# Optimization experiments

Measured on AMD Instinct MI355X. Metric: run time of the kernel, lower is better.

## Reference

```python
import jax, jax.numpy as jnp
import numpy as np

K1, K2 = 2, 4  # kernels of the two channel groups
BN_EPS = 1e-5


def _neocell_group(x, wa, wb, k):
    # Block-diagonal (a @ x) @ b with a k x k block repeated along the diagonal
    # per channel (NeoCellRepeat): equivalent to blockwise transforms on H and W.
    B, c, H, W = x.shape
    xb = x.reshape(B, c, H // k, k, W // k, k)
    y = jnp.einsum('cpi,bcnimj,cjq->bcnpmq', wa, xb, wb)
    return y.reshape(B, c, H, W)


def setup_inputs() -> dict:
    key = jax.random.key(0)
    ks = jax.random.split(key, 12)
    B, C, H, W = 32, 256, 56, 56
    c1, c2 = 128, 128
    Ci = 4 * C  # inner_mult = 4
    x = jax.random.normal(ks[0], (B, C, H, W), dtype=jnp.float32)
    wa1 = jax.random.normal(ks[1], (c1, K1, K1), dtype=jnp.float32) / np.float32(np.sqrt(K1))
    wb1 = jax.random.normal(ks[2], (c1, K1, K1), dtype=jnp.float32) / np.float32(np.sqrt(K1))
    wa2 = jax.random.normal(ks[3], (c2, K2, K2), dtype=jnp.float32) / np.float32(np.sqrt(K2))
    wb2 = jax.random.normal(ks[4], (c2, K2, K2), dtype=jnp.float32) / np.float32(np.sqrt(K2))
    bn_weight = 1.0 + 0.1 * jax.random.normal(ks[5], (C,), dtype=jnp.float32)
    bn_bias = 0.1 * jax.random.normal(ks[6], (C,), dtype=jnp.float32)
    bn_mean = 0.1 * jax.random.normal(ks[7], (C,), dtype=jnp.float32)
    bn_var = jax.random.uniform(ks[8], (C,), dtype=jnp.float32, minval=0.5, maxval=1.5)
    fc1_w = jax.random.normal(ks[9], (Ci, C), dtype=jnp.float32) / np.float32(np.sqrt(C))
    fc2_w = jax.random.normal(ks[10], (C, Ci), dtype=jnp.float32) / np.float32(np.sqrt(Ci))
    return {"x": x, "wa1": wa1, "wb1": wb1, "wa2": wa2, "wb2": wb2,
            "bn_weight": bn_weight, "bn_bias": bn_bias, "bn_mean": bn_mean,
            "bn_var": bn_var, "fc1_w": fc1_w, "fc2_w": fc2_w}


def reference(x, wa1, wb1, wa2, wb2, bn_weight, bn_bias, bn_mean, bn_var, fc1_w, fc2_w):
    c1 = wa1.shape[0]
    # NeoCell: per-group block-diagonal (a @ x) @ b
    y = jnp.concatenate([
        _neocell_group(x[:, :c1], wa1, wb1, K1),
        _neocell_group(x[:, c1:], wa2, wb2, K2),
    ], axis=1)
    # BatchNorm2d (eval mode, running stats)
    inv = jax.lax.rsqrt(bn_var + BN_EPS)
    scale = (bn_weight * inv)[None, :, None, None]
    shift = (bn_bias - bn_mean * bn_weight * inv)[None, :, None, None]
    y = y * scale + shift
    # chw -> hwc, MLP with exact GELU, hwc -> chw
    y = jnp.transpose(y, (0, 2, 3, 1))
    h = jax.nn.gelu(y @ fc1_w.T, approximate=False)
    y = h @ fc2_w.T
    y = jnp.transpose(y, (0, 3, 1, 2))
    # residual (drop_path = 0)
    return y + x
```

## Files before the change

### kernel.cpp

```cpp
#include <hip/hip_runtime.h>
#include <stdint.h>

typedef __bf16 bf16x8 __attribute__((ext_vector_type(8)));
typedef float f32x4 __attribute__((ext_vector_type(4)));

__device__ __forceinline__ float bf2f(uint16_t u) {
  union { uint32_t i; float f; } v; v.i = ((uint32_t)u) << 16; return v.f;
}
__device__ __forceinline__ uint16_t f2bf(float f) {
  union { float f; uint32_t i; } v; v.f = f;
  uint32_t u = v.i;
  uint32_t r = (u + 0x7FFFu + ((u >> 16) & 1u)) >> 16;
  return (uint16_t)r;
}

__global__ __launch_bounds__(256) void cvt_weights_kernel(
    const float* __restrict__ fc1, const float* __restrict__ fc2,
    uint16_t* __restrict__ fc1b, uint16_t* __restrict__ fc2b)
{
  int i = (blockIdx.x * 256 + threadIdx.x) * 4;
  if (i < 262144) {
    float4 a = *(const float4*)(fc1 + i);
    ushort4 o;
    o.x = f2bf(a.x); o.y = f2bf(a.y); o.z = f2bf(a.z); o.w = f2bf(a.w);
    *(ushort4*)(fc1b + i) = o;
  } else {
    int j = i - 262144;
    float4 a = *(const float4*)(fc2 + j);
    ushort4 o;
    o.x = f2bf(a.x); o.y = f2bf(a.y); o.z = f2bf(a.z); o.w = f2bf(a.w);
    *(ushort4*)(fc2b + j) = o;
  }
}

__global__ __launch_bounds__(128) void neocell_bn_kernel(
    const float* __restrict__ x,
    const float* __restrict__ wa1, const float* __restrict__ wb1,
    const float* __restrict__ wa2, const float* __restrict__ wb2,
    const float* __restrict__ bnw, const float* __restrict__ bnb,
    const float* __restrict__ bnm, const float* __restrict__ bnv,
    uint16_t* __restrict__ y1)
{
  __shared__ uint16_t lx[128 * 226];
  const int t = threadIdx.x;
  const int strip = blockIdx.x;
  const int b = blockIdx.y;
  const int half = blockIdx.z;
  const int h0 = strip * 4;

  for (int i = 0; i < 56; ++i) {
    int l = t + i * 128;
    int c = l / 56;
    int r = l - c * 56;
    const float* g = x + (size_t)(b * 256 + half * 128 + c) * 3136
                       + h0 * 56 + r * 4;
    float4 v = *(const float4*)g;
    ushort4 o;
    o.x = f2bf(v.x); o.y = f2bf(v.y); o.z = f2bf(v.z); o.w = f2bf(v.w);
    *(ushort4*)(lx + c * 226 + r * 4) = o;
  }
  __syncthreads();

  const int c = half * 128 + t;
  const float scale = bnw[c] * rsqrtf(bnv[c] + 1e-5f);
  const float shift = bnb[c] - bnm[c] * scale;
  const uint16_t* lc = lx + t * 226;
  const size_t prow0 = (size_t)b * 56;

  if (half == 0) {
    float A[2][2], Bm[2][2];
#pragma unroll
    for (int p = 0; p < 2; ++p)
#pragma unroll
      for (int i = 0; i < 2; ++i) A[p][i] = wa1[t * 4 + p * 2 + i];
#pragma unroll
    for (int j = 0; j < 2; ++j)
#pragma unroll
      for (int q = 0; q < 2; ++q) Bm[j][q] = wb1[t * 4 + j * 2 + q];

    for (int n2 = 0; n2 < 2; ++n2) {
      for (int m = 0; m < 28; ++m) {
        float X[2][2], T[2][2];
#pragma unroll
        for (int i = 0; i < 2; ++i)
#pragma unroll
          for (int j = 0; j < 2; ++j)
            X[i][j] = bf2f(lc[(n2 * 2 + i) * 56 + m * 2 + j]);
#pragma unroll
        for (int p = 0; p < 2; ++p)
#pragma unroll
          for (int j = 0; j < 2; ++j)
            T[p][j] = A[p][0] * X[0][j] + A[p][1] * X[1][j];
#pragma unroll
        for (int p = 0; p < 2; ++p)
#pragma unroll
          for (int q = 0; q < 2; ++q) {
            float v = T[p][0] * Bm[0][q] + T[p][1] * Bm[1][q];
            v = v * scale + shift;
            size_t pix = (prow0 + h0 + n2 * 2 + p) * 56 + (m * 2 + q);
            y1[pix * 256 + c] = f2bf(v);
          }
      }
    }
  } else {
    float A[4][4], Bm[4][4];
#pragma unroll
    for (int p = 0; p < 4; ++p)
#pragma unroll
      for (int i = 0; i < 4; ++i) A[p][i] = wa2[t * 16 + p * 4 + i];
#pragma unroll
    for (int j = 0; j < 4; ++j)
#pragma unroll
      for (int q = 0; q < 4; ++q) Bm[j][q] = wb2[t * 16 + j * 4 + q];

    for (int m = 0; m < 14; ++m) {
      float X[4][4], T[4][4];
#pragma unroll
      for (int i = 0; i < 4; ++i)
#pragma unroll
        for (int j = 0; j < 4; ++j)
          X[i][j] = bf2f(lc[i * 56 + m * 4 + j]);
#pragma unroll
      for (int p = 0; p < 4; ++p)
#pragma unroll
        for (int j = 0; j < 4; ++j)
          T[p][j] = A[p][0] * X[0][j] + A[p][1] * X[1][j]
                  + A[p][2] * X[2][j] + A[p][3] * X[3][j];
#pragma unroll
      for (int p = 0; p < 4; ++p)
#pragma unroll
        for (int q = 0; q < 4; ++q) {
          float v = T[p][0] * Bm[0][q] + T[p][1] * Bm[1][q]
                  + T[p][2] * Bm[2][q] + T[p][3] * Bm[3][q];
          v = v * scale + shift;
          size_t pix = (prow0 + h0 + p) * 56 + (m * 4 + q);
          y1[pix * 256 + c] = f2bf(v);
        }
    }
  }
}

template <int KD, int EPI>
__global__ __launch_bounds__(256) void gemm_bt_kernel(
    const uint16_t* __restrict__ A,
    const uint16_t* __restrict__ Bw,
    uint16_t* __restrict__ Cb16,
    float* __restrict__ Cf32,
    const float* __restrict__ Xres,
    int chunk_pix0)
{
  __shared__ uint16_t lds[16640];
  uint16_t* ldsA = lds;
  uint16_t* ldsB = lds + 4096;

  const int tid = threadIdx.x;
  const int lane = tid & 63;
  const int wid = tid >> 6;
  const int wm = wid & 1;
  const int wn = wid >> 1;
  const int fm = lane & 15;
  const int fq = lane >> 4;

  const size_t arow0 = (size_t)blockIdx.x * 128;
  const size_t brow0 = (size_t)blockIdx.y * 128;

  f32x4 acc[4][4];
#pragma unroll
  for (int i = 0; i < 4; ++i)
#pragma unroll
    for (int j = 0; j < 4; ++j) { f32x4 z = {0.f, 0.f, 0.f, 0.f}; acc[i][j] = z; }

  const int q0 = tid, q1 = tid + 256;
  const int r0 = q0 >> 2, kk0 = q0 & 3;
  const int r1 = q1 >> 2, kk1 = q1 & 3;
  const uint16_t* a0 = A + (arow0 + r0) * KD + kk0 * 8;
  const uint16_t* a1 = A + (arow0 + r1) * KD + kk1 * 8;
  const uint16_t* b0 = Bw + (brow0 + r0) * KD + kk0 * 8;
  const uint16_t* b1 = Bw + (brow0 + r1) * KD + kk1 * 8;

  for (int k0 = 0; k0 < KD; k0 += 32) {
    __syncthreads();
    __builtin_amdgcn_global_load_lds(
        (const __attribute__((address_space(1))) void*)(a0 + k0),
        (__attribute__((address_space(3))) void*)(ldsA + q0 * 8), 16, 0, 0);
    __builtin_amdgcn_global_load_lds(
        (const __attribute__((address_space(1))) void*)(a1 + k0),
        (__attribute__((address_space(3))) void*)(ldsA + q1 * 8), 16, 0, 0);
    __builtin_amdgcn_global_load_lds(
        (const __attribute__((address_space(1))) void*)(b0 + k0),
        (__attribute__((address_space(3))) void*)(ldsB + q0 * 8), 16, 0, 0);
    __builtin_amdgcn_global_load_lds(
        (const __attribute__((address_space(1))) void*)(b1 + k0),
        (__attribute__((address_space(3))) void*)(ldsB + q1 * 8), 16, 0, 0);
    __syncthreads();

    bf16x8 af[4], bfr[4];
#pragma unroll
    for (int mt = 0; mt < 4; ++mt)
      af[mt] = *(const bf16x8*)(const void*)
               (ldsA + (wm * 64 + mt * 16 + fm) * 32 + fq * 8);
#pragma unroll
    for (int nt = 0; nt < 4; ++nt)
      bfr[nt] = *(const bf16x8*)(const void*)
                (ldsB + (wn * 64 + nt * 16 + fm) * 32 + fq * 8);
#pragma unroll
    for (int mt = 0; mt < 4; ++mt)
#pragma unroll
      for (int nt = 0; nt < 4; ++nt)
        acc[mt][nt] = __builtin_amdgcn_mfma_f32_16x16x32_bf16(
            af[mt], bfr[nt], acc[mt][nt], 0, 0, 0);
  }

  if (EPI == 0) {
#pragma unroll
    for (int mt = 0; mt < 4; ++mt) {
      const size_t rb = arow0 + wm * 64 + mt * 16 + fq * 4;
#pragma unroll
      for (int nt = 0; nt < 4; ++nt) {
        const size_t n = brow0 + wn * 64 + nt * 16 + fm;
#pragma unroll
        for (int r = 0; r < 4; ++r) {
          float v = acc[mt][nt][r];
          v = 0.5f * v * (1.0f + erff(v * 0.70710678118654752f));
          Cb16[(rb + r) * 1024 + n] = f2bf(v);
        }
      }
    }
  } else {
    __syncthreads();
#pragma unroll
    for (int mt = 0; mt < 4; ++mt) {
      int mbase = wm * 64 + mt * 16 + fq * 4;
#pragma unroll
      for (int nt = 0; nt < 4; ++nt) {
        int n = wn * 64 + nt * 16 + fm;
#pragma unroll
        for (int r = 0; r < 4; ++r)
          lds[n * 130 + mbase + r] = f2bf(acc[mt][nt][r]);
      }
    }
    __syncthreads();
    const int pl0 = tid & 31;
    const int cw = tid >> 5;
#pragma unroll
    for (int it = 0; it < 16; ++it) {
      int ch = cw + it * 8;
      int cgl = (int)brow0 + ch;
#pragma unroll
      for (int e = 0; e < 4; ++e) {
        int pl = pl0 + e * 32;
        uint32_t pg = (uint32_t)(chunk_pix0) + blockIdx.x * 128u + (uint32_t)pl;
        uint32_t bimg = pg / 3136u;
        uint32_t rem = pg - bimg * 3136u;
        size_t addr = ((size_t)bimg * 256 + cgl) * 3136 + rem;
        Cf32[addr] = bf2f(lds[ch * 130 + pl]) + Xres[addr];
      }
    }
  }
}

extern "C" void kernel_launch(void* const* d_in, const int* in_sizes, int n_in,
                              void* d_out, int out_size, void* d_ws,
                              size_t ws_size, hipStream_t stream)
{
  const float* x   = (const float*)d_in[0];
  const float* wa1 = (const float*)d_in[1];
  const float* wb1 = (const float*)d_in[2];
  const float* wa2 = (const float*)d_in[3];
  const float* wb2 = (const float*)d_in[4];
  const float* bnw = (const float*)d_in[5];
  const float* bnb = (const float*)d_in[6];
  const float* bnm = (const float*)d_in[7];
  const float* bnv = (const float*)d_in[8];
  const float* fc1 = (const float*)d_in[9];
  const float* fc2 = (const float*)d_in[10];
  float* out = (float*)d_out;

  uint16_t* fc1b = (uint16_t*)d_ws;
  uint16_t* fc2b = fc1b + 262144;
  uint16_t* y1 = fc2b + 262144;
  const size_t y1_elems = (size_t)100352 * 256;
  uint16_t* h = y1 + y1_elems;

  const long tiles_total = 784;
  const size_t fixed_bytes = (size_t)262144 * 4 + y1_elems * 2;
  long tiles_chunk = 1;
  if (ws_size > fixed_bytes + 262144) {
    tiles_chunk = (long)((ws_size - fixed_bytes) / (128ul * 1024ul * 2ul));
    if (tiles_chunk > tiles_total) tiles_chunk = tiles_total;
    if (tiles_chunk < 1) tiles_chunk = 1;
  }

  cvt_weights_kernel<<<512, 256, 0, stream>>>(fc1, fc2, fc1b, fc2b);
  neocell_bn_kernel<<<dim3(14, 32, 2), 128, 0, stream>>>(
      x, wa1, wb1, wa2, wb2, bnw, bnb, bnm, bnv, y1);

  for (long t0 = 0; t0 < tiles_total; t0 += tiles_chunk) {
    long T = tiles_total - t0;
    if (T > tiles_chunk) T = tiles_chunk;
    gemm_bt_kernel<256, 0><<<dim3((uint32_t)T, 8), 256, 0, stream>>>(
        y1 + (size_t)t0 * 128 * 256, fc1b, h, nullptr, nullptr, 0);
    gemm_bt_kernel<1024, 1><<<dim3((uint32_t)T, 2), 256, 0, stream>>>(
        h, fc2b, nullptr, out, x, (int)(t0 * 128));
  }
}
```

Measured before the change: 496.3 us.

## Use fast GELU, pack two channels per neocell store, swap GEMM grid order

```diff
diff --git a/kernel.cpp b/kernel.cpp
--- a/kernel.cpp
+++ b/kernel.cpp
@@ -12,6 +12,13 @@
   uint32_t u = v.i;
   uint32_t r = (u + 0x7FFFu + ((u >> 16) & 1u)) >> 16;
   return (uint16_t)r;
+}
+__device__ __forceinline__ float fast_gelu(float v) {
+  float t2 = v * v;
+  float pz = 1.0f + 0.044715f * t2;
+  float w = -1.5957691216f * v * pz;
+  float e = __expf(w);
+  return v * __builtin_amdgcn_rcpf(1.0f + e);
 }
 
 __global__ __launch_bounds__(256) void cvt_weights_kernel(
@@ -61,80 +68,111 @@
   }
   __syncthreads();
 
-  const int c = half * 128 + t;
-  const float scale = bnw[c] * rsqrtf(bnv[c] + 1e-5f);
-  const float shift = bnb[c] - bnm[c] * scale;
-  const uint16_t* lc = lx + t * 226;
-  const size_t prow0 = (size_t)b * 56;
+  const int a = t & 63;
+  const int p = t >> 6;
+  const int c0 = half * 128 + 2 * a;
+
+  float sc[2], sh[2];
+#pragma unroll
+  for (int ch = 0; ch < 2; ++ch) {
+    int cg = c0 + ch;
+    sc[ch] = bnw[cg] * rsqrtf(bnv[cg] + 1e-5f);
+    sh[ch] = bnb[cg] - bnm[cg] * sc[ch];
+  }
+  const size_t pgbase = (size_t)b * 3136 + (size_t)h0 * 56;
 
   if (half == 0) {
-    float A[2][2], Bm[2][2];
-#pragma unroll
-    for (int p = 0; p < 2; ++p)
-#pragma unroll
-      for (int i = 0; i < 2; ++i) A[p][i] = wa1[t * 4 + p * 2 + i];
-#pragma unroll
-    for (int j = 0; j < 2; ++j)
-#pragma unroll
-      for (int q = 0; q < 2; ++q) Bm[j][q] = wb1[t * 4 + j * 2 + q];
-
-    for (int n2 = 0; n2 < 2; ++n2) {
-      for (int m = 0; m < 28; ++m) {
-        float X[2][2], T[2][2];
-#pragma unroll
-        for (int i = 0; i < 2; ++i)
+    float A[2][2][2], Bm[2][2][2];
+#pragma unroll
+    for (int ch = 0; ch < 2; ++ch)
+#pragma unroll
+      for (int i = 0; i < 2; ++i)
+#pragma unroll
+        for (int j = 0; j < 2; ++j) {
+          A[ch][i][j]  = wa1[(2 * a + ch) * 4 + i * 2 + j];
+          Bm[ch][i][j] = wb1[(2 * a + ch) * 4 + i * 2 + j];
+        }
+    for (int m = 0; m < 28; ++m) {
+      float O[2][2][2];
+#pragma unroll
+      for (int ch = 0; ch < 2; ++ch) {
+        const uint16_t* lc = lx + (2 * a + ch) * 226 + (2 * p) * 56 + m * 2;
+        uint32_t w0 = *(const uint32_t*)lc;
+        uint32_t w1 = *(const uint32_t*)(lc + 56);
+        float X[2][2];
+        X[0][0] = bf2f((uint16_t)w0); X[0][1] = bf2f((uint16_t)(w0 >> 16));
+        X[1][0] = bf2f((uint16_t)w1); X[1][1] = bf2f((uint16_t)(w1 >> 16));
+        float T[2][2];
+#pragma unroll
+        for (int pp = 0; pp < 2; ++pp)
 #pragma unroll
           for (int j = 0; j < 2; ++j)
-            X[i][j] = bf2f(lc[(n2 * 2 + i) * 56 + m * 2 + j]);
-#pragma unroll
-        for (int p = 0; p < 2; ++p)
-#pragma unroll
-          for (int j = 0; j < 2; ++j)
-            T[p][j] = A[p][0] * X[0][j] + A[p][1] * X[1][j];
-#pragma unroll
-        for (int p = 0; p < 2; ++p)
-#pragma unroll
-          for (int q = 0; q < 2; ++q) {
-            float v = T[p][0] * Bm[0][q] + T[p][1] * Bm[1][q];
-            v = v * scale + shift;
-            size_t pix = (prow0 + h0 + n2 * 2 + p) * 56 + (m * 2 + q);
-            y1[pix * 256 + c] = f2bf(v);
-          }
-      }
+            T[pp][j] = A[ch][pp][0] * X[0][j] + A[ch][pp][1] * X[1][j];
+#pragma unroll
+        for (int pp = 0; pp < 2; ++pp)
+#pragma unroll
+          for (int q = 0; q < 2; ++q)
+            O[ch][pp][q] = (T[pp][0] * Bm[ch][0][q] + T[pp][1] * Bm[ch][1][q])
+                           * sc[ch] + sh[ch];
+      }
+#pragma unroll
+      for (int pp = 0; pp < 2; ++pp)
+#pragma unroll
+        for (int q = 0; q < 2; ++q) {
+          uint32_t pk = (uint32_t)f2bf(O[0][pp][q])
+                      | ((uint32_t)f2bf(O[1][pp][q]) << 16);
+          size_t pg = pgbase + (size_t)(2 * p + pp) * 56 + (m * 2 + q);
+          *(uint32_t*)(y1 + pg * 256 + c0) = pk;
+        }
     }
   } else {
-    float A[4][4], Bm[4][4];
-#pragma unroll
-    for (int p = 0; p < 4; ++p)
-#pragma unroll
-      for (int i = 0; i < 4; ++i) A[p][i] = wa2[t * 16 + p * 4 + i];
-#pragma unroll
-    for (int j = 0; j < 4; ++j)
-#pragma unroll
-      for (int q = 0; q < 4; ++q) Bm[j][q] = wb2[t * 16 + j * 4 + q];
-
-    for (int m = 0; m < 14; ++m) {
-      float X[4][4], T[4][4];
+    float A[2][4][4], Bm[2][4][4];
+#pragma unroll
+    for (int ch = 0; ch < 2; ++ch)
 #pragma unroll
       for (int i = 0; i < 4; ++i)
 #pragma unroll
-        for (int j = 0; j < 4; ++j)
-          X[i][j] = bf2f(lc[i * 56 + m * 4 + j]);
-#pragma unroll
-      for (int p = 0; p < 4; ++p)
-#pragma unroll
-        for (int j = 0; j < 4; ++j)
-          T[p][j] = A[p][0] * X[0][j] + A[p][1] * X[1][j]
-                  + A[p][2] * X[2][j] + A[p][3] * X[3][j];
-#pragma unroll
-      for (int p = 0; p < 4; ++p)
+        for (int j = 0; j < 4; ++j) {
+          A[ch][i][j]  = wa2[(2 * a + ch) * 16 + i * 4 + j];
+          Bm[ch][i][j] = wb2[(2 * a + ch) * 16 + i * 4 + j];
+        }
+    for (int mm = 0; mm < 7; ++mm) {
+      int m = 2 * mm + p;
+      float O[2][4][4];
+#pragma unroll
+      for (int ch = 0; ch < 2; ++ch) {
+        float X[4][4];
+#pragma unroll
+        for (int i = 0; i < 4; ++i) {
+          const uint16_t* lc = lx + (2 * a + ch) * 226 + i * 56 + m * 4;
+          uint32_t w0 = *(const uint32_t*)lc;
+          uint32_t w1 = *(const uint32_t*)(lc + 2);
+          X[i][0] = bf2f((uint16_t)w0); X[i][1] = bf2f((uint16_t)(w0 >> 16));
+          X[i][2] = bf2f((uint16_t)w1); X[i][3] = bf2f((uint16_t)(w1 >> 16));
+        }
+        float T[4][4];
+#pragma unroll
+        for (int pp = 0; pp < 4; ++pp)
+#pragma unroll
+          for (int j = 0; j < 4; ++j)
+            T[pp][j] = A[ch][pp][0] * X[0][j] + A[ch][pp][1] * X[1][j]
+                     + A[ch][pp][2] * X[2][j] + A[ch][pp][3] * X[3][j];
+#pragma unroll
+        for (int pp = 0; pp < 4; ++pp)
+#pragma unroll
+          for (int q = 0; q < 4; ++q)
+            O[ch][pp][q] = (T[pp][0] * Bm[ch][0][q] + T[pp][1] * Bm[ch][1][q]
+                          + T[pp][2] * Bm[ch][2][q] + T[pp][3] * Bm[ch][3][q])
+                           * sc[ch] + sh[ch];
+      }
+#pragma unroll
+      for (int pp = 0; pp < 4; ++pp)
 #pragma unroll
         for (int q = 0; q < 4; ++q) {
-          float v = T[p][0] * Bm[0][q] + T[p][1] * Bm[1][q]
-                  + T[p][2] * Bm[2][q] + T[p][3] * Bm[3][q];
-          v = v * scale + shift;
-          size_t pix = (prow0 + h0 + p) * 56 + (m * 4 + q);
-          y1[pix * 256 + c] = f2bf(v);
+          uint32_t pk = (uint32_t)f2bf(O[0][pp][q])
+                      | ((uint32_t)f2bf(O[1][pp][q]) << 16);
+          size_t pg = pgbase + (size_t)pp * 56 + (m * 4 + q);
+          *(uint32_t*)(y1 + pg * 256 + c0) = pk;
         }
     }
   }
@@ -161,8 +199,8 @@
   const int fm = lane & 15;
   const int fq = lane >> 4;
 
-  const size_t arow0 = (size_t)blockIdx.x * 128;
-  const size_t brow0 = (size_t)blockIdx.y * 128;
+  const size_t arow0 = (size_t)blockIdx.y * 128;
+  const size_t brow0 = (size_t)blockIdx.x * 128;
 
   f32x4 acc[4][4];
 #pragma unroll
@@ -219,11 +257,8 @@
       for (int nt = 0; nt < 4; ++nt) {
         const size_t n = brow0 + wn * 64 + nt * 16 + fm;
 #pragma unroll
-        for (int r = 0; r < 4; ++r) {
-          float v = acc[mt][nt][r];
-          v = 0.5f * v * (1.0f + erff(v * 0.70710678118654752f));
-          Cb16[(rb + r) * 1024 + n] = f2bf(v);
-        }
+        for (int r = 0; r < 4; ++r)
+          Cb16[(rb + r) * 1024 + n] = f2bf(fast_gelu(acc[mt][nt][r]));
       }
     }
   } else {
@@ -249,7 +284,7 @@
 #pragma unroll
       for (int e = 0; e < 4; ++e) {
         int pl = pl0 + e * 32;
-        uint32_t pg = (uint32_t)(chunk_pix0) + blockIdx.x * 128u + (uint32_t)pl;
+        uint32_t pg = (uint32_t)chunk_pix0 + blockIdx.y * 128u + (uint32_t)pl;
         uint32_t bimg = pg / 3136u;
         uint32_t rem = pg - bimg * 3136u;
         size_t addr = ((size_t)bimg * 256 + cgl) * 3136 + rem;
@@ -298,9 +333,9 @@
   for (long t0 = 0; t0 < tiles_total; t0 += tiles_chunk) {
     long T = tiles_total - t0;
     if (T > tiles_chunk) T = tiles_chunk;
-    gemm_bt_kernel<256, 0><<<dim3((uint32_t)T, 8), 256, 0, stream>>>(
+    gemm_bt_kernel<256, 0><<<dim3(8, (uint32_t)T), 256, 0, stream>>>(
         y1 + (size_t)t0 * 128 * 256, fc1b, h, nullptr, nullptr, 0);
-    gemm_bt_kernel<1024, 1><<<dim3((uint32_t)T, 2), 256, 0, stream>>>(
+    gemm_bt_kernel<1024, 1><<<dim3(2, (uint32_t)T), 256, 0, stream>>>(
         h, fc2b, nullptr, out, x, (int)(t0 * 128));
   }
 }
```

New measurement: 443.1 us. 10.7% less time.
